# Kernel optimization log

Hardware: AMD Instinct MI355X
Metric: run time of the kernel (lower is better)

Reference implementation:

```python
import jax, jax.numpy as jnp
import numpy as np

B_J0 = 0.01
BETA = 1.8
GAMMA = 0.5
LENS = 0.5
TAU_M = 20.0
DT = 1.0
IN_SIZE = 4
FULL_LEN = 784
T_STEPS = FULL_LEN // IN_SIZE  # 196 sequential steps
H1, H2, H3 = 512, 512, 512
OUT = 10
BATCH = 256


@jax.custom_vjp
def spike_fn(x):
    # ActFun_adp: heaviside forward, rectangular surrogate backward
    return (x > 0).astype(x.dtype)

def _spike_fwd(x):
    return (x > 0).astype(x.dtype), x

def _spike_bwd(x, g):
    return (GAMMA * g * (jnp.abs(x) < LENS).astype(g.dtype),)

spike_fn.defvjp(_spike_fwd, _spike_bwd)


def _make_mask(dim, c_min, c_max, min_dc, max_dc, phase_max, T=784):
    # Faithful port of create_general_mask
    dc_steps = np.linspace(min_dc, max_dc, dim)
    cycles = np.linspace(c_min, c_max, dim)
    phases = np.linspace(0.0, float(int(phase_max * c_max)), dim)
    rows = []
    for cyc, dc, ph in zip(cycles, dc_steps, phases):
        cyc = int(np.ceil(cyc))
        on = int(np.ceil(dc * cyc))
        pat = [1] * on + [0] * (cyc - on)
        p = int(np.round(ph))
        if p > 0:
            pat = pat[-p:] + pat[:-p]
        rows.append(pat * (T // cyc) + pat[: T % cyc])
    return jnp.asarray(np.array(rows, dtype=np.float32))


def setup_inputs() -> dict:
    key = jax.random.key(0)
    ks = jax.random.split(key, 8)

    def xav(k, o, i):
        return jax.random.normal(k, (o, i), jnp.float32) * np.float32(np.sqrt(2.0 / (o + i)))

    return {
        "x": jax.random.uniform(ks[0], (BATCH, FULL_LEN), jnp.float32),
        "W_i2h1": xav(ks[1], H1, IN_SIZE), "b_i2h1": jnp.zeros(H1, jnp.float32),
        "W_h2h1": xav(ks[2], H1, H1), "b_h2h1": jnp.zeros(H1, jnp.float32),
        "W_i2h2": xav(ks[3], H2, H1), "b_i2h2": jnp.zeros(H2, jnp.float32),
        "W_h2h2": xav(ks[4], H2, H2), "b_h2h2": jnp.zeros(H2, jnp.float32),
        "W_i2h3": xav(ks[5], H3, H2), "b_i2h3": jnp.zeros(H3, jnp.float32),
        "W_h2o": xav(ks[6], OUT, H3), "b_h2o": jnp.zeros(OUT, jnp.float32),
        "tau_adp_h1": jnp.full((H1,), 700.0, jnp.float32),
        "tau_adp_h2": jnp.full((H2,), 700.0, jnp.float32),
        "tau_adp_h3": jnp.full((H3,), 700.0, jnp.float32),
        "mask1": _make_mask(H1, 2, 10, 0.1, 0.9, 0.5),
        "mask2": _make_mask(H2, 2, 10, 0.1, 0.9, 0.5),
        "mask3": _make_mask(H3, 2, 10, 0.1, 0.9, 0.5),
    }


def _forward(x, params, mask1, mask2, mask3):
    (W_i2h1, b_i2h1, W_h2h1, b_h2h1, W_i2h2, b_i2h2, W_h2h2, b_h2h2,
     W_i2h3, b_i2h3, W_h2o, b_h2o, tau1, tau2, tau3) = params
    N = x.shape[0]
    # Faithful to torch: condition uses self.T (196), not 784, so most steps
    # reuse the last IN_SIZE columns.
    cols = np.stack([
        np.arange(s * IN_SIZE, s * IN_SIZE + IN_SIZE)
        if s * IN_SIZE < T_STEPS - IN_SIZE
        else np.arange(FULL_LEN - IN_SIZE, FULL_LEN)
        for s in range(T_STEPS)
    ])
    x_seq = jnp.transpose(x[:, cols], (1, 0, 2))  # (T, N, IN)
    alpha = jnp.exp(jnp.float32(-DT / TAU_M))
    ro1 = jnp.exp(-DT / tau1)
    ro2 = jnp.exp(-DT / tau2)
    ro3 = jnp.exp(-DT / tau3)
    m1_seq = mask1[:, :T_STEPS].T  # (T, H1)
    m2_seq = mask2[:, :T_STEPS].T
    m3_seq = mask3[:, :T_STEPS].T

    def upd(inputs, mem, spk, ro, b, mask):
        # mem_update_NU_adp_skip, isAdapt=1
        b = ro * b + (1.0 - ro) * spk
        Bth = B_J0 + BETA * b
        new_mem = mem * alpha + (1.0 - alpha) * inputs - Bth * spk * DT
        mem = jnp.where(mask == 0, mem, new_mem)
        spk = spike_fn(mem - Bth) * mask
        return mem, spk, b

    def step(carry, xs):
        mem1, s1, bb1, mem2, s2, bb2, mem3, s3, bb3, acc = carry
        x_t, mk1, mk2, mk3 = xs
        h1 = x_t @ W_i2h1.T + b_i2h1 + s1 @ W_h2h1.T + b_h2h1
        mem1, s1, bb1 = upd(h1, mem1, s1, ro1, bb1, mk1)
        h2 = s1 @ W_i2h2.T + b_i2h2 + s2 @ W_h2h2.T + b_h2h2
        mem2, s2, bb2 = upd(h2, mem2, s2, ro2, bb2, mk2)
        h3 = s2 @ W_i2h3.T + b_i2h3
        mem3, s3, bb3 = upd(h3, mem3, s3, ro3, bb3, mk3)
        acc = acc + s3 @ W_h2o.T + b_h2o
        return (mem1, s1, bb1, mem2, s2, bb2, mem3, s3, bb3, acc), None

    z = lambda h: jnp.zeros((N, h), x.dtype)
    bj = lambda h: jnp.full((N, h), B_J0, x.dtype)  # b starts at scalar b_j0
    carry0 = (z(H1), z(H1), bj(H1), z(H2), z(H2), bj(H2), z(H3), z(H3), bj(H3), z(OUT))
    carry, _ = jax.lax.scan(step, carry0, (x_seq, m1_seq, m2_seq, m3_seq))
    return carry[-1] / T_STEPS


def reference(x, W_i2h1, b_i2h1, W_h2h1, b_h2h1, W_i2h2, b_i2h2, W_h2h2, b_h2h2,
              W_i2h3, b_i2h3, W_h2o, b_h2o, tau_adp_h1, tau_adp_h2, tau_adp_h3,
              mask1, mask2, mask3):
    params = (W_i2h1, b_i2h1, W_h2h1, b_h2h1, W_i2h2, b_i2h2, W_h2h2, b_h2h2,
              W_i2h3, b_i2h3, W_h2o, b_h2o, tau_adp_h1, tau_adp_h2, tau_adp_h3)
    return _forward(x, params, mask1, mask2, mask3)
```

## Files before the change

### kernel.cpp

```cpp
#include <hip/hip_runtime.h>

#define H 512
#define TSTEPS 196
#define FLEN 784
#define NBATCH 256

typedef float f4 __attribute__((ext_vector_type(4)));


__global__ void transpose4(const float* __restrict__ a,
                           const float* __restrict__ b,
                           const float* __restrict__ c,
                           const float* __restrict__ d,
                           float* __restrict__ ws)
{
    __shared__ float tile[32][33];
    const float* src = (blockIdx.z == 0) ? a : (blockIdx.z == 1) ? b
                     : (blockIdx.z == 2) ? c : d;
    float* dst = ws + (size_t)blockIdx.z * (H * H);
    int bx = blockIdx.x * 32, by = blockIdx.y * 32;
    int tx = threadIdx.x, ty = threadIdx.y;
    for (int r = ty; r < 32; r += 8)
        tile[r][tx] = src[(by + r) * H + bx + tx];
    __syncthreads();
    for (int r = ty; r < 32; r += 8)
        dst[(bx + r) * H + by + tx] = tile[tx][r];
}

__global__ void maskT3(const float* __restrict__ m1, const float* __restrict__ m2,
                       const float* __restrict__ m3, float* __restrict__ mt)
{
    int idx = blockIdx.x * 256 + threadIdx.x;
    if (idx >= TSTEPS * H) return;
    const float* src = (blockIdx.z == 0) ? m1 : (blockIdx.z == 1) ? m2 : m3;
    float* dst = mt + (size_t)blockIdx.z * (TSTEPS * H);
    int t = idx >> 9, j = idx & (H - 1);
    dst[idx] = src[j * FLEN + t];
}

__device__ __forceinline__ f4 gatherq(const float* __restrict__ WTq,
                                      const int* __restrict__ list,
                                      int lo, int hi)
{
    f4 a0 = (f4)0.0f, a1 = (f4)0.0f, a2 = (f4)0.0f, a3 = (f4)0.0f;
    int i = lo;
    for (; i + 4 <= hi; i += 4) {
        int k0 = list[i], k1 = list[i + 1], k2 = list[i + 2], k3 = list[i + 3];
        a0 += *(const f4*)(WTq + k0);
        a1 += *(const f4*)(WTq + k1);
        a2 += *(const f4*)(WTq + k2);
        a3 += *(const f4*)(WTq + k3);
    }
    for (; i < hi; ++i)
        a0 += *(const f4*)(WTq + list[i]);
    return (a0 + a1) + (a2 + a3);
}

__device__ __forceinline__ float sumg(const float* __restrict__ p, int j, int ng)
{
    float s = 0.0f;
    for (int gg = 0; gg < ng; ++gg)
        s += p[gg * H + j];
    return s;
}

__global__ __launch_bounds__(1024)
void lsnn_main(const float* __restrict__ x,
               const float* __restrict__ Wi1,
               const float* __restrict__ bi1, const float* __restrict__ bh1,
               const float* __restrict__ bi2, const float* __restrict__ bh2,
               const float* __restrict__ bi3,
               const float* __restrict__ Wo,  const float* __restrict__ bo,
               const float* __restrict__ tau1, const float* __restrict__ tau2,
               const float* __restrict__ tau3,
               const float* __restrict__ ws,
               float* __restrict__ out)
{
    const float* m1T = ws + 1048576;
    const float* m2T = m1T + TSTEPS * H;
    const float* m3T = m2T + TSTEPS * H;

    const int n    = blockIdx.x;
    const int tid  = threadIdx.x;
    const int j    = tid & (H - 1);
    const int lane = tid & 63;
    const int wid8 = (tid >> 6) & 7;
    const bool upd = tid < 512;
    const int u    = tid & 127;
    const int g    = tid >> 7;
    const int q4   = g & 3;

    const float* WT1q  = ws +           (u << 2);
    const float* WTi2q = ws + 262144 + (u << 2);
    const float* WTh2q = ws + 524288 + (u << 2);
    const float* WTi3q = ws + 786432 + (u << 2);

    __shared__ int list1[H], list2[H];
    __shared__ f4  part[3][8][128];
    __shared__ f4  pH[4][128];
    __shared__ int wcnt[8];

    float4 wi = reinterpret_cast<const float4*>(Wi1)[j];
    float bs1 = bi1[j] + bh1[j];
    float bs2 = bi2[j] + bh2[j];
    float bs3 = bi3[j];
    float ro1 = expf(-1.0f / tau1[j]);
    float ro2 = expf(-1.0f / tau2[j]);
    float ro3 = expf(-1.0f / tau3[j]);
    float omr1 = 1.0f - ro1, omr2 = 1.0f - ro2, omr3 = 1.0f - ro3;
    const float alpha = expf(-1.0f / 20.0f);
    const float oma = 1.0f - alpha;

    float mem1 = 0.f, mem2 = 0.f, mem3 = 0.f;
    float b1 = 0.01f, b2 = 0.01f, b3 = 0.01f;
    float s1 = 0.f, s2 = 0.f, s3 = 0.f;
    float cnt3 = 0.f;
    int na1 = 0, na2 = 0;

    const float* xr = x + n * FLEN;

    for (int t = 0; t < TSTEPS; ++t) {
        {
            int ch = (na1 + 7) >> 3;
            int lo = g * ch; lo = lo < na1 ? lo : na1;
            int hi = lo + ch; hi = hi < na1 ? hi : na1;
            part[0][g][u] = gatherq(WT1q, list1, lo, hi);
        }
        __syncthreads();
        unsigned long long ball = 0;
        if (upd) {
            int base = (t < 48) ? (4 * t) : (FLEN - 4);
            float4 xv = *reinterpret_cast<const float4*>(xr + base);
            float mk1 = m1T[t * H + j];
            float h1 = wi.x * xv.x + wi.y * xv.y + wi.z * xv.z + wi.w * xv.w
                     + bs1 + sumg((const float*)&part[0][0][0], j, 8);
            b1 = ro1 * b1 + omr1 * s1;
            float Bth = 0.01f + 1.8f * b1;
            float nm = mem1 * alpha + oma * h1 - Bth * s1;
            mem1 = (mk1 == 0.0f) ? mem1 : nm;
            s1 = (mem1 - Bth > 0.0f) ? mk1 : 0.0f;
            ball = __ballot(s1 != 0.0f);
            if (lane == 0) wcnt[wid8] = __popcll(ball);
        } else {
            int ch = (na2 + 3) >> 2;
            int lo = q4 * ch; lo = lo < na2 ? lo : na2;
            int hi = lo + ch; hi = hi < na2 ? hi : na2;
            pH[q4][u] = gatherq(WTh2q, list2, lo, hi);
        }
        __syncthreads();
        {
            int basew = 0, tot = 0;
#pragma unroll
            for (int w = 0; w < 8; ++w) {
                int c = wcnt[w];
                if (w < wid8) basew += c;
                tot += c;
            }
            if (upd && s1 != 0.0f) {
                int pre = __popcll(ball & ((1ull << lane) - 1ull));
                list1[basew + pre] = j << 9;
            }
            na1 = tot;
        }
        __syncthreads();

        {
            int ch = (na1 + 7) >> 3;
            int lo = g * ch; lo = lo < na1 ? lo : na1;
            int hi = lo + ch; hi = hi < na1 ? hi : na1;
            part[1][g][u] = gatherq(WTi2q, list1, lo, hi);
        }
        __syncthreads();
        if (upd) {
            float mk2 = m2T[t * H + j];
            float h2 = bs2 + sumg((const float*)&part[1][0][0], j, 8)
                           + sumg((const float*)&pH[0][0], j, 4);
            b2 = ro2 * b2 + omr2 * s2;
            float Bth = 0.01f + 1.8f * b2;
            float nm = mem2 * alpha + oma * h2 - Bth * s2;
            mem2 = (mk2 == 0.0f) ? mem2 : nm;
            s2 = (mem2 - Bth > 0.0f) ? mk2 : 0.0f;
            ball = __ballot(s2 != 0.0f);
            if (lane == 0) wcnt[wid8] = __popcll(ball);
        }
        __syncthreads();
        {
            int basew = 0, tot = 0;
#pragma unroll
            for (int w = 0; w < 8; ++w) {
                int c = wcnt[w];
                if (w < wid8) basew += c;
                tot += c;
            }
            if (upd && s2 != 0.0f) {
                int pre = __popcll(ball & ((1ull << lane) - 1ull));
                list2[basew + pre] = j << 9;
            }
            na2 = tot;
        }
        __syncthreads();

        {
            int ch = (na2 + 7) >> 3;
            int lo = g * ch; lo = lo < na2 ? lo : na2;
            int hi = lo + ch; hi = hi < na2 ? hi : na2;
            part[2][g][u] = gatherq(WTi3q, list2, lo, hi);
        }
        __syncthreads();
        if (upd) {
            float mk3 = m3T[t * H + j];
            float h3 = bs3 + sumg((const float*)&part[2][0][0], j, 8);
            b3 = ro3 * b3 + omr3 * s3;
            float Bth = 0.01f + 1.8f * b3;
            float nm = mem3 * alpha + oma * h3 - Bth * s3;
            mem3 = (mk3 == 0.0f) ? mem3 : nm;
            s3 = (mem3 - Bth > 0.0f) ? mk3 : 0.0f;
            cnt3 += s3;
        }
    }

    __syncthreads();
    float* c3 = (float*)&part[0][0][0];
    if (upd) c3[j] = cnt3;
    __syncthreads();
    int wv = tid >> 6;
    for (int o = wv; o < 10; o += 16) {
        float p = 0.0f;
        for (int i = lane; i < H; i += 64)
            p += Wo[o * H + i] * c3[i];
        for (int off = 32; off > 0; off >>= 1)
            p += __shfl_down(p, off);
        if (lane == 0)
            out[n * 10 + o] = (p + 196.0f * bo[o]) / 196.0f;
    }
}

extern "C" void kernel_launch(void* const* d_in, const int* in_sizes, int n_in,
                              void* d_out, int out_size, void* d_ws, size_t ws_size,
                              hipStream_t stream)
{
    const float* x    = (const float*)d_in[0];
    const float* Wi1  = (const float*)d_in[1];
    const float* bi1  = (const float*)d_in[2];
    const float* Wh1  = (const float*)d_in[3];
    const float* bh1  = (const float*)d_in[4];
    const float* Wi2  = (const float*)d_in[5];
    const float* bi2  = (const float*)d_in[6];
    const float* Wh2  = (const float*)d_in[7];
    const float* bh2  = (const float*)d_in[8];
    const float* Wi3  = (const float*)d_in[9];
    const float* bi3  = (const float*)d_in[10];
    const float* Wo   = (const float*)d_in[11];
    const float* bo   = (const float*)d_in[12];
    const float* tau1 = (const float*)d_in[13];
    const float* tau2 = (const float*)d_in[14];
    const float* tau3 = (const float*)d_in[15];
    const float* m1   = (const float*)d_in[16];
    const float* m2   = (const float*)d_in[17];
    const float* m3   = (const float*)d_in[18];

    float* ws  = (float*)d_ws;
    float* out = (float*)d_out;

    transpose4<<<dim3(16, 16, 4), dim3(32, 8, 1), 0, stream>>>(Wh1, Wi2, Wh2, Wi3, ws);
    maskT3<<<dim3((TSTEPS * H + 255) / 256, 1, 3), 256, 0, stream>>>(m1, m2, m3, ws + 1048576);

    lsnn_main<<<NBATCH, 1024, 0, stream>>>(x, Wi1, bi1, bh1, bi2, bh2, bi3,
                                           Wo, bo, tau1, tau2, tau3, ws, out);
}
```

Before: 741.7 us.

## Replace spike lists with ballot bitmasks and skew layer 3 one step to cut barriers

Spike lists built by prefix-sum compaction are replaced with per-wave ballot bitmasks kept in shared memory. Each thread group walks its byte of the mask with ctz to gather transposed weight columns. Layer 3's update is delayed by one timestep so its gather runs in the same phase as the layer-1 and recurrent layer-2 gathers, which drops the barriers per step from seven to four. Masks are precomputed as bit arrays rather than transposed floats. The trade-offs are an uneven split of work across groups when spikes cluster and one extra loop iteration.

New measurement: 917.3 us. 23.7% more time.

```diff
diff --git a/kernel.cpp b/kernel.cpp
--- a/kernel.cpp
+++ b/kernel.cpp
@@ -6,7 +6,9 @@
 #define NBATCH 256
 
 typedef float f4 __attribute__((ext_vector_type(4)));
-
+typedef unsigned long long ull;
+
+#define MBOFF_F 1048576
 
 __global__ void transpose4(const float* __restrict__ a,
                            const float* __restrict__ b,
@@ -27,41 +29,49 @@
         dst[(bx + r) * H + by + tx] = tile[tx][r];
 }
 
-__global__ void maskT3(const float* __restrict__ m1, const float* __restrict__ m2,
-                       const float* __restrict__ m3, float* __restrict__ mt)
-{
-    int idx = blockIdx.x * 256 + threadIdx.x;
-    if (idx >= TSTEPS * H) return;
-    const float* src = (blockIdx.z == 0) ? m1 : (blockIdx.z == 1) ? m2 : m3;
-    float* dst = mt + (size_t)blockIdx.z * (TSTEPS * H);
-    int t = idx >> 9, j = idx & (H - 1);
-    dst[idx] = src[j * FLEN + t];
-}
-
-__device__ __forceinline__ f4 gatherq(const float* __restrict__ WTq,
-                                      const int* __restrict__ list,
-                                      int lo, int hi)
-{
-    f4 a0 = (f4)0.0f, a1 = (f4)0.0f, a2 = (f4)0.0f, a3 = (f4)0.0f;
-    int i = lo;
-    for (; i + 4 <= hi; i += 4) {
-        int k0 = list[i], k1 = list[i + 1], k2 = list[i + 2], k3 = list[i + 3];
-        a0 += *(const f4*)(WTq + k0);
-        a1 += *(const f4*)(WTq + k1);
-        a2 += *(const f4*)(WTq + k2);
-        a3 += *(const f4*)(WTq + k3);
-    }
-    for (; i < hi; ++i)
-        a0 += *(const f4*)(WTq + list[i]);
-    return (a0 + a1) + (a2 + a3);
-}
-
-__device__ __forceinline__ float sumg(const float* __restrict__ p, int j, int ng)
-{
-    float s = 0.0f;
-    for (int gg = 0; gg < ng; ++gg)
-        s += p[gg * H + j];
-    return s;
+__global__ void maskbits(const float* __restrict__ m1, const float* __restrict__ m2,
+                         const float* __restrict__ m3, ull* __restrict__ mb)
+{
+    int t = blockIdx.x;
+    int z = blockIdx.y;
+    int l = threadIdx.x;
+    const float* src = (z == 0) ? m1 : (z == 1) ? m2 : m3;
+    for (int w = 0; w < 8; ++w) {
+        ull bl = __ballot(src[(w * 64 + l) * FLEN + t] != 0.0f);
+        if (l == 0) mb[(size_t)z * (TSTEPS * 8) + t * 8 + w] = bl;
+    }
+}
+
+__device__ __forceinline__ f4 gjob(const char* __restrict__ wsb, unsigned moff,
+                                   const unsigned char* __restrict__ bb, int g)
+{
+    f4 a0 = (f4)0.0f, a1 = (f4)0.0f;
+#pragma unroll
+    for (int w = 0; w < 8; ++w) {
+        unsigned b = bb[w * 8 + g];
+        unsigned cbase = moff + (((unsigned)(w * 64 + g * 8)) << 11);
+        while (b) {
+            int k = __builtin_ctz(b);
+            b &= b - 1;
+            f4 v = *(const f4*)(wsb + (cbase + ((unsigned)k << 11)));
+            if (w & 1) a1 += v; else a0 += v;
+        }
+    }
+    return a0 + a1;
+}
+
+__device__ __forceinline__ float sum8(const float* __restrict__ p, int j)
+{
+    float s0 = p[j] + p[512 + j];
+    float s1 = p[1024 + j] + p[1536 + j];
+    float s2 = p[2048 + j] + p[2560 + j];
+    float s3 = p[3072 + j] + p[3584 + j];
+    return (s0 + s1) + (s2 + s3);
+}
+
+__device__ __forceinline__ float mbit(const ull* __restrict__ mb, int t, int j)
+{
+    return ((mb[t * 8 + (j >> 6)] >> (j & 63)) & 1ull) ? 1.0f : 0.0f;
 }
 
 __global__ __launch_bounds__(1024)
@@ -76,9 +86,10 @@
                const float* __restrict__ ws,
                float* __restrict__ out)
 {
-    const float* m1T = ws + 1048576;
-    const float* m2T = m1T + TSTEPS * H;
-    const float* m3T = m2T + TSTEPS * H;
+    const char* wsb = (const char*)ws;
+    const ull* mb1 = (const ull*)(ws + MBOFF_F);
+    const ull* mb2 = mb1 + TSTEPS * 8;
+    const ull* mb3 = mb2 + TSTEPS * 8;
 
     const int n    = blockIdx.x;
     const int tid  = threadIdx.x;
@@ -88,17 +99,19 @@
     const bool upd = tid < 512;
     const int u    = tid & 127;
     const int g    = tid >> 7;
-    const int q4   = g & 3;
-
-    const float* WT1q  = ws +           (u << 2);
-    const float* WTi2q = ws + 262144 + (u << 2);
-    const float* WTh2q = ws + 524288 + (u << 2);
-    const float* WTi3q = ws + 786432 + (u << 2);
-
-    __shared__ int list1[H], list2[H];
-    __shared__ f4  part[3][8][128];
-    __shared__ f4  pH[4][128];
-    __shared__ int wcnt[8];
+
+    const unsigned uoff  = (unsigned)u << 4;
+    const unsigned OFF_H1 = (0u << 20) + uoff;
+    const unsigned OFF_I2 = (1u << 20) + uoff;
+    const unsigned OFF_H2 = (2u << 20) + uoff;
+    const unsigned OFF_I3 = (3u << 20) + uoff;
+
+    __shared__ f4  partA[8][128];
+    __shared__ f4  partB[8][128];
+    __shared__ f4  partC[8][128];
+    __shared__ ull ballS[16];
+    const unsigned char* bb1 = (const unsigned char*)&ballS[0];
+    const unsigned char* bb2 = (const unsigned char*)&ballS[8];
 
     float4 wi = reinterpret_cast<const float4*>(Wi1)[j];
     float bs1 = bi1[j] + bh1[j];
@@ -115,112 +128,74 @@
     float b1 = 0.01f, b2 = 0.01f, b3 = 0.01f;
     float s1 = 0.f, s2 = 0.f, s3 = 0.f;
     float cnt3 = 0.f;
-    int na1 = 0, na2 = 0;
 
     const float* xr = x + n * FLEN;
 
-    for (int t = 0; t < TSTEPS; ++t) {
+    if (tid < 16) ballS[tid] = 0ull;
+    __syncthreads();
+
+    for (int t = 0; t <= TSTEPS; ++t) {
         {
-            int ch = (na1 + 7) >> 3;
-            int lo = g * ch; lo = lo < na1 ? lo : na1;
-            int hi = lo + ch; hi = hi < na1 ? hi : na1;
-            part[0][g][u] = gatherq(WT1q, list1, lo, hi);
-        }
-        __syncthreads();
-        unsigned long long ball = 0;
+            f4 aG3 = gjob(wsb, OFF_I3, bb2, g);
+            f4 aG1 = (f4)0.0f, aH = (f4)0.0f;
+            if (t < TSTEPS) {
+                aG1 = gjob(wsb, OFF_H1, bb1, g);
+                aH  = gjob(wsb, OFF_H2, bb2, g);
+            }
+            partA[g][u] = aG1;
+            partB[g][u] = aG3;
+            partC[g][u] = aH;
+        }
+        __syncthreads();
+
         if (upd) {
-            int base = (t < 48) ? (4 * t) : (FLEN - 4);
-            float4 xv = *reinterpret_cast<const float4*>(xr + base);
-            float mk1 = m1T[t * H + j];
-            float h1 = wi.x * xv.x + wi.y * xv.y + wi.z * xv.z + wi.w * xv.w
-                     + bs1 + sumg((const float*)&part[0][0][0], j, 8);
-            b1 = ro1 * b1 + omr1 * s1;
-            float Bth = 0.01f + 1.8f * b1;
-            float nm = mem1 * alpha + oma * h1 - Bth * s1;
-            mem1 = (mk1 == 0.0f) ? mem1 : nm;
-            s1 = (mem1 - Bth > 0.0f) ? mk1 : 0.0f;
-            ball = __ballot(s1 != 0.0f);
-            if (lane == 0) wcnt[wid8] = __popcll(ball);
-        } else {
-            int ch = (na2 + 3) >> 2;
-            int lo = q4 * ch; lo = lo < na2 ? lo : na2;
-            int hi = lo + ch; hi = hi < na2 ? hi : na2;
-            pH[q4][u] = gatherq(WTh2q, list2, lo, hi);
-        }
-        __syncthreads();
-        {
-            int basew = 0, tot = 0;
-#pragma unroll
-            for (int w = 0; w < 8; ++w) {
-                int c = wcnt[w];
-                if (w < wid8) basew += c;
-                tot += c;
+            if (t > 0) {
+                float mk3 = mbit(mb3, t - 1, j);
+                float h3 = bs3 + sum8((const float*)&partB[0][0], j);
+                b3 = ro3 * b3 + omr3 * s3;
+                float Bth = 0.01f + 1.8f * b3;
+                float nm = mem3 * alpha + oma * h3 - Bth * s3;
+                mem3 = (mk3 == 0.0f) ? mem3 : nm;
+                s3 = (mem3 - Bth > 0.0f) ? mk3 : 0.0f;
+                cnt3 += s3;
             }
-            if (upd && s1 != 0.0f) {
-                int pre = __popcll(ball & ((1ull << lane) - 1ull));
-                list1[basew + pre] = j << 9;
+            if (t < TSTEPS) {
+                float mk1 = mbit(mb1, t, j);
+                int base = (t < 48) ? (4 * t) : (FLEN - 4);
+                float4 xv = *reinterpret_cast<const float4*>(xr + base);
+                float h1 = wi.x * xv.x + wi.y * xv.y + wi.z * xv.z + wi.w * xv.w
+                         + bs1 + sum8((const float*)&partA[0][0], j);
+                b1 = ro1 * b1 + omr1 * s1;
+                float Bth = 0.01f + 1.8f * b1;
+                float nm = mem1 * alpha + oma * h1 - Bth * s1;
+                mem1 = (mk1 == 0.0f) ? mem1 : nm;
+                s1 = (mem1 - Bth > 0.0f) ? mk1 : 0.0f;
+                ull ball = __ballot(s1 != 0.0f);
+                if (lane == 0) ballS[wid8] = ball;
             }
-            na1 = tot;
-        }
-        __syncthreads();
-
-        {
-            int ch = (na1 + 7) >> 3;
-            int lo = g * ch; lo = lo < na1 ? lo : na1;
-            int hi = lo + ch; hi = hi < na1 ? hi : na1;
-            part[1][g][u] = gatherq(WTi2q, list1, lo, hi);
-        }
-        __syncthreads();
-        if (upd) {
-            float mk2 = m2T[t * H + j];
-            float h2 = bs2 + sumg((const float*)&part[1][0][0], j, 8)
-                           + sumg((const float*)&pH[0][0], j, 4);
+        }
+        __syncthreads();
+
+        if (t < TSTEPS)
+            partA[g][u] = gjob(wsb, OFF_I2, bb1, g);
+        __syncthreads();
+
+        if (upd && t < TSTEPS) {
+            float mk2 = mbit(mb2, t, j);
+            float h2 = bs2 + sum8((const float*)&partA[0][0], j)
+                           + sum8((const float*)&partC[0][0], j);
             b2 = ro2 * b2 + omr2 * s2;
             float Bth = 0.01f + 1.8f * b2;
             float nm = mem2 * alpha + oma * h2 - Bth * s2;
             mem2 = (mk2 == 0.0f) ? mem2 : nm;
             s2 = (mem2 - Bth > 0.0f) ? mk2 : 0.0f;
-            ball = __ballot(s2 != 0.0f);
-            if (lane == 0) wcnt[wid8] = __popcll(ball);
-        }
-        __syncthreads();
-        {
-            int basew = 0, tot = 0;
-#pragma unroll
-            for (int w = 0; w < 8; ++w) {
-                int c = wcnt[w];
-                if (w < wid8) basew += c;
-                tot += c;
-            }
-            if (upd && s2 != 0.0f) {
-                int pre = __popcll(ball & ((1ull << lane) - 1ull));
-                list2[basew + pre] = j << 9;
-            }
-            na2 = tot;
-        }
-        __syncthreads();
-
-        {
-            int ch = (na2 + 7) >> 3;
-            int lo = g * ch; lo = lo < na2 ? lo : na2;
-            int hi = lo + ch; hi = hi < na2 ? hi : na2;
-            part[2][g][u] = gatherq(WTi3q, list2, lo, hi);
-        }
-        __syncthreads();
-        if (upd) {
-            float mk3 = m3T[t * H + j];
-            float h3 = bs3 + sumg((const float*)&part[2][0][0], j, 8);
-            b3 = ro3 * b3 + omr3 * s3;
-            float Bth = 0.01f + 1.8f * b3;
-            float nm = mem3 * alpha + oma * h3 - Bth * s3;
-            mem3 = (mk3 == 0.0f) ? mem3 : nm;
-            s3 = (mem3 - Bth > 0.0f) ? mk3 : 0.0f;
-            cnt3 += s3;
-        }
-    }
-
-    __syncthreads();
-    float* c3 = (float*)&part[0][0][0];
+            ull ball = __ballot(s2 != 0.0f);
+            if (lane == 0) ballS[8 + wid8] = ball;
+        }
+        __syncthreads();
+    }
+
+    float* c3 = (float*)&partA[0][0];
     if (upd) c3[j] = cnt3;
     __syncthreads();
     int wv = tid >> 6;
@@ -263,7 +238,7 @@
     float* out = (float*)d_out;
 
     transpose4<<<dim3(16, 16, 4), dim3(32, 8, 1), 0, stream>>>(Wh1, Wi2, Wh2, Wi3, ws);
-    maskT3<<<dim3((TSTEPS * H + 255) / 256, 1, 3), 256, 0, stream>>>(m1, m2, m3, ws + 1048576);
+    maskbits<<<dim3(TSTEPS, 3, 1), 64, 0, stream>>>(m1, m2, m3, (ull*)(ws + MBOFF_F));
 
     lsnn_main<<<NBATCH, 1024, 0, stream>>>(x, Wi1, bi1, bh1, bi2, bh2, bi3,
                                            Wo, bo, tau1, tau2, tau3, ws, out);
```
